# Kernel optimization log

Measured on AMD Instinct MI355X. Metric: run time of the kernel, lower is better.

The kernel has to match this reference:

```python
import jax, jax.numpy as jnp
import numpy as np

B, C, H, W = 4, 128, 64, 64


def setup_inputs() -> dict:
    key = jax.random.key(0)
    ks = jax.random.split(key, 7)
    s = 1.0 / np.sqrt(C)
    return {
        "x": jax.random.normal(ks[0], (B, C, H, W), dtype=jnp.float32),
        "Wq": jax.random.normal(ks[1], (C, C), dtype=jnp.float32) * s,
        "bq": jnp.zeros((C,), dtype=jnp.float32),
        "Wk": jax.random.normal(ks[2], (C, C), dtype=jnp.float32) * s,
        "bk": jnp.zeros((C,), dtype=jnp.float32),
        "Wv": jax.random.normal(ks[3], (C, C), dtype=jnp.float32) * s,
        "bv": jnp.zeros((C,), dtype=jnp.float32),
    }


def reference(x, Wq, bq, Wk, bk, Wv, bv):
    b, c, h, w = x.shape
    n = h * w
    scale = c ** (-0.5)
    # tokens: [B, N, C]
    xt = x.reshape(b, c, n).transpose(0, 2, 1)
    # 1x1 convs == per-token channel GEMMs (out[c'] = sum_c W[c',c] x[c] + b[c'])
    q = jnp.einsum("bnc,dc->bnd", xt, Wq) + bq  # [B, N, C]
    k = jnp.einsum("bnc,dc->bnd", xt, Wk) + bk  # [B, N, C]
    v = jnp.einsum("bnc,dc->bnd", xt, Wv) + bv  # [B, N, C]
    scores = jnp.einsum("bic,bjc->bij", q, k) * scale  # [B, N, N]
    attn = jax.nn.softmax(scores, axis=-1)
    out = jnp.einsum("bij,bjc->bic", attn, v)  # [B, N, C]
    return out.transpose(0, 2, 1).reshape(b, c, h, w)
```

## Files before the change

kernel.cpp:

```cpp
#include <hip/hip_runtime.h>
#include <hip/hip_bf16.h>


#define BATCH 4
#define CH    128
#define NTOK  4096
#define SCALE 0.08838834764831845f
#define LOG2E 1.4426950408889634f
#define MFIX  16.0f

typedef __attribute__((ext_vector_type(8)))  short short8;
typedef __attribute__((ext_vector_type(4)))  float f32x4;
typedef __attribute__((ext_vector_type(16))) float f32x16;

static __device__ __forceinline__ unsigned short f2bf(float f) {
    __hip_bfloat16 h = (__hip_bfloat16)f;
    return *(const unsigned short*)&h;
}

static __device__ __forceinline__ unsigned cvt_pk_bf16(float lo, float hi) {
    unsigned r;
    asm("v_cvt_pk_bf16_f32 %0, %1, %2" : "=v"(r) : "v"(lo), "v"(hi));
    return r;
}

static __device__ __forceinline__ short8 pack_bf16x8(float4 a, float4 b) {
    union { unsigned u[4]; short8 s8; } f;
    f.u[0] = cvt_pk_bf16(a.x, a.y);
    f.u[1] = cvt_pk_bf16(a.z, a.w);
    f.u[2] = cvt_pk_bf16(b.x, b.y);
    f.u[3] = cvt_pk_bf16(b.z, b.w);
    return f.s8;
}

__global__ __launch_bounds__(256) void proj_mfma_kernel(
    const float* __restrict__ x,
    const float* __restrict__ Wq, const float* __restrict__ Wk,
    const float* __restrict__ Wv,
    const float* __restrict__ bq, const float* __restrict__ bk,
    const float* __restrict__ bv,
    unsigned short* __restrict__ q_ws, unsigned short* __restrict__ kf_ws,
    unsigned short* __restrict__ vf_ws)
{
    __shared__ __align__(16) unsigned short Wl[CH * CH];
    __shared__ __align__(16) unsigned short XsT[64 * CH];

    const int t    = threadIdx.x;
    const int w    = t >> 6;
    const int lane = t & 63;
    const int quad = lane >> 4;
    const int c16  = lane & 15;
    const int n0   = blockIdx.x * 64;
    const int b    = blockIdx.y;
    const int z    = blockIdx.z;
    const float* xb = x + (size_t)b * CH * NTOK;
    const float* wm = (z == 0) ? Wq : (z == 1) ? Wk : Wv;

    #pragma unroll
    for (int i = 0; i < 8; ++i) {
        const int f   = i * 256 + t;
        const int row = f >> 4;
        const int u   = f & 15;
        const float* src = wm + f * 8;
        const float4 a = *(const float4*)src;
        const float4 c = *(const float4*)(src + 4);
        *(short8*)&Wl[row * CH + ((u ^ (row & 15)) << 3)] = pack_bf16x8(a, c);
    }
    {
        const int tok = lane;
        #pragma unroll
        for (int cc = 0; cc < 4; ++cc) {
            const int cb = 32 * w + 8 * cc;
            float xv[8];
            #pragma unroll
            for (int j = 0; j < 8; ++j)
                xv[j] = xb[(size_t)(cb + j) * NTOK + n0 + tok];
            union { unsigned u[4]; short8 s8; } pk;
            #pragma unroll
            for (int j = 0; j < 4; ++j)
                pk.u[j] = cvt_pk_bf16(xv[2 * j], xv[2 * j + 1]);
            const int phys = ((cb >> 3) ^ (tok & 15));
            *(short8*)&XsT[tok * CH + phys * 8] = pk.s8;
        }
    }
    __syncthreads();

    if (z < 2) {
        const float* bias = (z == 0) ? bq : bk;
        const float mul = (z == 0) ? (SCALE * LOG2E) : 1.0f;
        short8 xa[4];
        #pragma unroll
        for (int ks = 0; ks < 4; ++ks)
            xa[ks] = *(const short8*)&XsT[(16 * w + c16) * CH + (((4 * ks + quad) ^ c16) << 3)];
        #pragma unroll
        for (int nt = 0; nt < 8; ++nt) {
            f32x4 a = (f32x4){0.f, 0.f, 0.f, 0.f};
            #pragma unroll
            for (int ks = 0; ks < 4; ++ks) {
                const short8 bf = *(const short8*)
                    &Wl[(16 * nt + c16) * CH + (((4 * ks + quad) ^ c16) << 3)];
                a = __builtin_amdgcn_mfma_f32_16x16x32_bf16(xa[ks], bf, a, 0, 0, 0);
            }
            const float bvv = bias[16 * nt + c16];
            #pragma unroll
            for (int r = 0; r < 4; ++r) {
                const int n = n0 + 16 * w + quad * 4 + r;
                if (z == 0) {
                    q_ws[((size_t)b * NTOK + n) * CH + 16 * nt + c16] =
                        f2bf((a[r] + bvv) * mul);
                } else {
                    const size_t idx =
                        (((size_t)b * (NTOK >> 5) + (n >> 5)) * 8 + nt) * 512
                        + ((n & 31) + 32 * (c16 >> 3)) * 8 + (c16 & 7);
                    kf_ws[idx] = f2bf(a[r] + bvv);
                }
            }
        }
    } else {
        #pragma unroll
        for (int nt = 0; nt < 4; ++nt) {
            short8 xbf[4];
            #pragma unroll
            for (int ks = 0; ks < 4; ++ks)
                xbf[ks] = *(const short8*)&XsT[(16 * nt + c16) * CH + (((4 * ks + quad) ^ c16) << 3)];
            #pragma unroll
            for (int mt = 0; mt < 2; ++mt) {
                const int crow16 = 16 * (2 * w + mt);
                f32x4 acc = (f32x4){0.f, 0.f, 0.f, 0.f};
                #pragma unroll
                for (int ks = 0; ks < 4; ++ks) {
                    const short8 wva = *(const short8*)
                        &Wl[(crow16 + c16) * CH + (((4 * ks + quad) ^ c16) << 3)];
                    acc = __builtin_amdgcn_mfma_f32_16x16x32_bf16(wva, xbf[ks], acc, 0, 0, 0);
                }
                #pragma unroll
                for (int r = 0; r < 4; ++r) {
                    const int ch  = crow16 + quad * 4 + r;
                    const int tok = n0 + 16 * nt + c16;
                    const size_t idx =
                        ((((size_t)b * (NTOK >> 5) + (tok >> 5)) * 2
                          + ((tok >> 4) & 1)) * 4 + (ch >> 5)) * 512
                        + ((ch & 31) + 32 * ((tok >> 3) & 1)) * 8 + (tok & 7);
                    vf_ws[idx] = f2bf(acc[r] + bv[ch]);
                }
            }
        }
    }
}

template <int SPLIT>
__global__ __launch_bounds__(256, 2) void flash_attn_mfma(
    const unsigned short* __restrict__ q_ws,
    const unsigned short* __restrict__ kf_ws,
    const unsigned short* __restrict__ vf_ws,
    float* __restrict__ out,
    float* __restrict__ Op, float* __restrict__ l_p)
{
    const int t    = threadIdx.x;
    const int w    = t >> 6;
    const int lane = t & 63;
    const int half = lane >> 5;
    const int l32  = lane & 31;

    int xx, jc, b;
    if constexpr (SPLIT % 2 == 0) {
        const int bid = blockIdx.x;
        b = (bid & 7) >> 1;
        const int sub = (bid & 1) * (16 * SPLIT) + (bid >> 3);
        jc = sub >> 5;
        xx = sub & 31;
    } else {
        const int bid = blockIdx.x;
        xx = bid & 31;
        jc = 0;
        b  = bid >> 5;
    }

    const int n0   = xx * 128;
    const int jbeg = jc * (NTOK / SPLIT);
    constexpr int NT2 = (NTOK / SPLIT) / 32;

    const unsigned short* kg = kf_ws + (size_t)b * NTOK * CH;
    const unsigned short* vg = vf_ws + (size_t)b * NTOK * CH;

    short8 qa[8];
    {
        const unsigned short* qrow =
            q_ws + ((size_t)b * NTOK + n0 + 32 * w + l32) * CH;
        #pragma unroll
        for (int ks = 0; ks < 8; ++ks)
            qa[ks] = *(const short8*)(qrow + ks * 16 + half * 8);
    }

    f32x16 Oa[4];
    #pragma unroll
    for (int ct = 0; ct < 4; ++ct) Oa[ct] = (f32x16)(0.0f);
    float lsum = 0.f;

    short8 kf[8];
    auto KF_LOAD = [&](int jj) {
        const unsigned short* kb = kg + (size_t)(jj >> 5) * (8 * 512);
        #pragma unroll
        for (int ks = 0; ks < 8; ++ks)
            kf[ks] = *(const short8*)(kb + (ks * 64 + lane) * 8);
    };

    KF_LOAD(jbeg);

    int j0 = jbeg;
    for (int tt = 0; tt < NT2; ++tt, j0 += 32) {
        f32x16 s = (f32x16)(-MFIX);
        #pragma unroll
        for (int ks = 0; ks < 8; ++ks)
            s = __builtin_amdgcn_mfma_f32_32x32x16_bf16(kf[ks], qa[ks], s, 0, 0, 0);

        short8 vfA[4], vfB[4];
        {
            const unsigned short* vb = vg + (size_t)(j0 >> 5) * (8 * 512);
            #pragma unroll
            for (int ct = 0; ct < 4; ++ct)
                vfA[ct] = *(const short8*)(vb + ((0 * 4 + ct) * 64 + lane) * 8);
            #pragma unroll
            for (int ct = 0; ct < 4; ++ct)
                vfB[ct] = *(const short8*)(vb + ((1 * 4 + ct) * 64 + lane) * 8);
        }
        if (tt + 1 < NT2) KF_LOAD(j0 + 32);

        float p[16];
        #pragma unroll
        for (int r = 0; r < 16; ++r) p[r] = exp2f(s[r]);
        {
            float a0 = 0.f, a1 = 0.f, a2 = 0.f, a3 = 0.f;
            #pragma unroll
            for (int r = 0; r < 4; ++r) {
                a0 += p[r]; a1 += p[4 + r]; a2 += p[8 + r]; a3 += p[12 + r];
            }
            lsum += (a0 + a1) + (a2 + a3);
        }
        short8 pb0, pb1;
        {
            unsigned wd[8];
            #pragma unroll
            for (int i = 0; i < 8; ++i) wd[i] = cvt_pk_bf16(p[2 * i], p[2 * i + 1]);
            auto r02 = __builtin_amdgcn_permlane32_swap(wd[0], wd[2], false, false);
            auto r13 = __builtin_amdgcn_permlane32_swap(wd[1], wd[3], false, false);
            auto r46 = __builtin_amdgcn_permlane32_swap(wd[4], wd[6], false, false);
            auto r57 = __builtin_amdgcn_permlane32_swap(wd[5], wd[7], false, false);
            union { unsigned u[4]; short8 s8; } f0, f1;
            f0.u[0] = r02[0]; f0.u[1] = r13[0]; f0.u[2] = r02[1]; f0.u[3] = r13[1];
            f1.u[0] = r46[0]; f1.u[1] = r57[0]; f1.u[2] = r46[1]; f1.u[3] = r57[1];
            pb0 = f0.s8;
            pb1 = f1.s8;
        }

        #pragma unroll
        for (int ct = 0; ct < 4; ++ct)
            Oa[ct] = __builtin_amdgcn_mfma_f32_32x32x16_bf16(vfA[ct], pb0, Oa[ct], 0, 0, 0);
        #pragma unroll
        for (int ct = 0; ct < 4; ++ct)
            Oa[ct] = __builtin_amdgcn_mfma_f32_32x32x16_bf16(vfB[ct], pb1, Oa[ct], 0, 0, 0);
    }

    const float lt = lsum + __shfl_xor(lsum, 32);
    const int n = n0 + 32 * w + l32;

    if constexpr (SPLIT == 1) {
        const float inv = 1.0f / lt;
        #pragma unroll
        for (int ct = 0; ct < 4; ++ct) {
            #pragma unroll
            for (int r = 0; r < 16; ++r) {
                const int c = 32 * ct + (r & 3) + 8 * (r >> 2) + 4 * half;
                out[((size_t)b * CH + c) * NTOK + n] = Oa[ct][r] * inv;
            }
        }
    } else {
        const size_t chunk = (size_t)(b * SPLIT + jc);
        #pragma unroll
        for (int ct = 0; ct < 4; ++ct) {
            #pragma unroll
            for (int r = 0; r < 16; ++r) {
                const int c = 32 * ct + (r & 3) + 8 * (r >> 2) + 4 * half;
                Op[(chunk * CH + c) * NTOK + n] = Oa[ct][r];
            }
        }
        if (half == 0) l_p[chunk * NTOK + n] = lt;
    }
}

template <int SPLIT>
__global__ __launch_bounds__(256) void combine_kernel(
    const float* __restrict__ Op, const float* __restrict__ l_p,
    float* __restrict__ out)
{
    const int b = blockIdx.y;
    const size_t idx = ((size_t)blockIdx.x * 256 + threadIdx.x) * 4;
    const int c = (int)(idx >> 12);
    const int n = (int)(idx & (NTOK - 1));
    float4 acc = make_float4(0.f, 0.f, 0.f, 0.f);
    float4 den = make_float4(0.f, 0.f, 0.f, 0.f);
    #pragma unroll
    for (int j = 0; j < SPLIT; ++j) {
        const size_t chunk = (size_t)(b * SPLIT + j);
        const float4 o = *(const float4*)&Op[(chunk * CH + c) * NTOK + n];
        const float4 d = *(const float4*)&l_p[chunk * NTOK + n];
        acc.x += o.x; acc.y += o.y; acc.z += o.z; acc.w += o.w;
        den.x += d.x; den.y += d.y; den.z += d.z; den.w += d.w;
    }
    float4 r;
    r.x = acc.x / den.x; r.y = acc.y / den.y;
    r.z = acc.z / den.z; r.w = acc.w / den.w;
    *(float4*)&out[((size_t)b * CH * NTOK) + idx] = r;
}

extern "C" void kernel_launch(void* const* d_in, const int* in_sizes, int n_in,
                              void* d_out, int out_size, void* d_ws, size_t ws_size,
                              hipStream_t stream) {
    const float* x  = (const float*)d_in[0];
    const float* Wq = (const float*)d_in[1];
    const float* bq = (const float*)d_in[2];
    const float* Wk = (const float*)d_in[3];
    const float* bk = (const float*)d_in[4];
    const float* Wv = (const float*)d_in[5];
    const float* bv = (const float*)d_in[6];
    float* out = (float*)d_out;

    const size_t QKV = (size_t)BATCH * NTOK * CH;
    unsigned short* q_ws  = (unsigned short*)d_ws;
    unsigned short* kf_ws = q_ws + QKV;
    unsigned short* vf_ws = kf_ws + QKV;
    float* Op = (float*)(vf_ws + QKV);

    const size_t baseBytes = 3 * QKV * 2;
    auto needBytes = [&](size_t S) {
        return baseBytes + S * BATCH * NTOK * (size_t)(CH * 4 + 4);
    };

    dim3 gp(NTOK / 64, BATCH, 3);
    proj_mfma_kernel<<<gp, 256, 0, stream>>>(x, Wq, Wk, Wv, bq, bk, bv,
                                             q_ws, kf_ws, vf_ws);

    dim3 gc(CH * NTOK / 1024, BATCH);
    if (ws_size >= needBytes(8)) {
        float* l_p = Op + (size_t)8 * BATCH * NTOK * CH;
        flash_attn_mfma<8><<<dim3(128 * 8), 256, 0, stream>>>(
            q_ws, kf_ws, vf_ws, out, Op, l_p);
        combine_kernel<8><<<gc, 256, 0, stream>>>(Op, l_p, out);
    } else if (ws_size >= needBytes(4)) {
        float* l_p = Op + (size_t)4 * BATCH * NTOK * CH;
        flash_attn_mfma<4><<<dim3(128 * 4), 256, 0, stream>>>(
            q_ws, kf_ws, vf_ws, out, Op, l_p);
        combine_kernel<4><<<gc, 256, 0, stream>>>(Op, l_p, out);
    } else {
        flash_attn_mfma<1><<<dim3(32 * BATCH), 256, 0, stream>>>(
            q_ws, kf_ws, vf_ws, out, nullptr, nullptr);
    }
}
```

Measured before the change: 132.1 us.

## Process two query subtiles per wave to double K/V reuse, stage Q in LDS

Each wave now computes attention for 64 queries (two 32-row subtiles) instead of 32, so each loaded K and V fragment feeds twice as many MFMAs. Q fragments move from registers to shared memory to offset the doubled output accumulators. The second subtile's QK^T and softmax are interleaved with the first's to overlap work. The grid is halved accordingly; this raises register pressure and adds LDS reads, and may reduce occupancy or block-level parallelism.

```diff
diff --git a/kernel.cpp b/kernel.cpp
--- a/kernel.cpp
+++ b/kernel.cpp
@@ -156,6 +156,8 @@
     float* __restrict__ out,
     float* __restrict__ Op, float* __restrict__ l_p)
 {
+    __shared__ __align__(16) unsigned short Ql[4 * 2 * 8 * 64 * 8];
+
     const int t    = threadIdx.x;
     const int w    = t >> 6;
     const int lane = t & 63;
@@ -166,36 +168,41 @@
     if constexpr (SPLIT % 2 == 0) {
         const int bid = blockIdx.x;
         b = (bid & 7) >> 1;
-        const int sub = (bid & 1) * (16 * SPLIT) + (bid >> 3);
-        jc = sub >> 5;
-        xx = sub & 31;
+        const int sub = (bid & 1) * (8 * SPLIT) + (bid >> 3);
+        jc = sub >> 4;
+        xx = sub & 15;
     } else {
-        const int bid = blockIdx.x;
-        xx = bid & 31;
+        xx = blockIdx.x & 15;
         jc = 0;
-        b  = bid >> 5;
-    }
-
-    const int n0   = xx * 128;
+        b  = blockIdx.x >> 4;
+    }
+
+    const int n0   = xx * 256;
     const int jbeg = jc * (NTOK / SPLIT);
     constexpr int NT2 = (NTOK / SPLIT) / 32;
 
     const unsigned short* kg = kf_ws + (size_t)b * NTOK * CH;
     const unsigned short* vg = vf_ws + (size_t)b * NTOK * CH;
 
-    short8 qa[8];
     {
-        const unsigned short* qrow =
-            q_ws + ((size_t)b * NTOK + n0 + 32 * w + l32) * CH;
-        #pragma unroll
-        for (int ks = 0; ks < 8; ++ks)
-            qa[ks] = *(const short8*)(qrow + ks * 16 + half * 8);
-    }
-
-    f32x16 Oa[4];
+        const unsigned short* qbase =
+            q_ws + ((size_t)b * NTOK + n0 + 64 * w) * CH;
+        #pragma unroll
+        for (int qs = 0; qs < 2; ++qs)
+            #pragma unroll
+            for (int ks = 0; ks < 8; ++ks) {
+                const short8 v = *(const short8*)
+                    (qbase + (qs * 32 + l32) * CH + ks * 16 + half * 8);
+                *(short8*)&Ql[(((w * 2 + qs) * 8 + ks) * 64 + lane) * 8] = v;
+            }
+    }
+
+    f32x16 Oa[2][4];
     #pragma unroll
-    for (int ct = 0; ct < 4; ++ct) Oa[ct] = (f32x16)(0.0f);
-    float lsum = 0.f;
+    for (int qs = 0; qs < 2; ++qs)
+        #pragma unroll
+        for (int ct = 0; ct < 4; ++ct) Oa[qs][ct] = (f32x16)(0.0f);
+    float lsum[2] = {0.f, 0.f};
 
     short8 kf[8];
     auto KF_LOAD = [&](int jj) {
@@ -204,15 +211,44 @@
         for (int ks = 0; ks < 8; ++ks)
             kf[ks] = *(const short8*)(kb + (ks * 64 + lane) * 8);
     };
+    auto QKT = [&](int qs, f32x16& s) {
+        #pragma unroll
+        for (int ks = 0; ks < 8; ++ks) {
+            const short8 qf = *(const short8*)
+                &Ql[(((w * 2 + qs) * 8 + ks) * 64 + lane) * 8];
+            s = __builtin_amdgcn_mfma_f32_32x32x16_bf16(kf[ks], qf, s, 0, 0, 0);
+        }
+    };
+    auto SOFTMAX = [&](int qs, const f32x16& s, short8& pb0, short8& pb1) {
+        float p[16];
+        #pragma unroll
+        for (int r = 0; r < 16; ++r) p[r] = exp2f(s[r]);
+        float a0 = 0.f, a1 = 0.f, a2 = 0.f, a3 = 0.f;
+        #pragma unroll
+        for (int r = 0; r < 4; ++r) {
+            a0 += p[r]; a1 += p[4 + r]; a2 += p[8 + r]; a3 += p[12 + r];
+        }
+        lsum[qs] += (a0 + a1) + (a2 + a3);
+        unsigned wd[8];
+        #pragma unroll
+        for (int i = 0; i < 8; ++i) wd[i] = cvt_pk_bf16(p[2 * i], p[2 * i + 1]);
+        auto r02 = __builtin_amdgcn_permlane32_swap(wd[0], wd[2], false, false);
+        auto r13 = __builtin_amdgcn_permlane32_swap(wd[1], wd[3], false, false);
+        auto r46 = __builtin_amdgcn_permlane32_swap(wd[4], wd[6], false, false);
+        auto r57 = __builtin_amdgcn_permlane32_swap(wd[5], wd[7], false, false);
+        union { unsigned u[4]; short8 s8; } f0, f1;
+        f0.u[0] = r02[0]; f0.u[1] = r13[0]; f0.u[2] = r02[1]; f0.u[3] = r13[1];
+        f1.u[0] = r46[0]; f1.u[1] = r57[0]; f1.u[2] = r46[1]; f1.u[3] = r57[1];
+        pb0 = f0.s8;
+        pb1 = f1.s8;
+    };
 
     KF_LOAD(jbeg);
 
     int j0 = jbeg;
     for (int tt = 0; tt < NT2; ++tt, j0 += 32) {
-        f32x16 s = (f32x16)(-MFIX);
-        #pragma unroll
-        for (int ks = 0; ks < 8; ++ks)
-            s = __builtin_amdgcn_mfma_f32_32x32x16_bf16(kf[ks], qa[ks], s, 0, 0, 0);
+        f32x16 s0 = (f32x16)(-MFIX);
+        QKT(0, s0);
 
         short8 vfA[4], vfB[4];
         {
@@ -224,67 +260,56 @@
             for (int ct = 0; ct < 4; ++ct)
                 vfB[ct] = *(const short8*)(vb + ((1 * 4 + ct) * 64 + lane) * 8);
         }
+
+        short8 pb00, pb01;
+        SOFTMAX(0, s0, pb00, pb01);
+
+        f32x16 s1 = (f32x16)(-MFIX);
+        QKT(1, s1);
         if (tt + 1 < NT2) KF_LOAD(j0 + 32);
 
-        float p[16];
-        #pragma unroll
-        for (int r = 0; r < 16; ++r) p[r] = exp2f(s[r]);
-        {
-            float a0 = 0.f, a1 = 0.f, a2 = 0.f, a3 = 0.f;
-            #pragma unroll
-            for (int r = 0; r < 4; ++r) {
-                a0 += p[r]; a1 += p[4 + r]; a2 += p[8 + r]; a3 += p[12 + r];
-            }
-            lsum += (a0 + a1) + (a2 + a3);
-        }
-        short8 pb0, pb1;
-        {
-            unsigned wd[8];
-            #pragma unroll
-            for (int i = 0; i < 8; ++i) wd[i] = cvt_pk_bf16(p[2 * i], p[2 * i + 1]);
-            auto r02 = __builtin_amdgcn_permlane32_swap(wd[0], wd[2], false, false);
-            auto r13 = __builtin_amdgcn_permlane32_swap(wd[1], wd[3], false, false);
-            auto r46 = __builtin_amdgcn_permlane32_swap(wd[4], wd[6], false, false);
-            auto r57 = __builtin_amdgcn_permlane32_swap(wd[5], wd[7], false, false);
-            union { unsigned u[4]; short8 s8; } f0, f1;
-            f0.u[0] = r02[0]; f0.u[1] = r13[0]; f0.u[2] = r02[1]; f0.u[3] = r13[1];
-            f1.u[0] = r46[0]; f1.u[1] = r57[0]; f1.u[2] = r46[1]; f1.u[3] = r57[1];
-            pb0 = f0.s8;
-            pb1 = f1.s8;
-        }
-
-        #pragma unroll
-        for (int ct = 0; ct < 4; ++ct)
-            Oa[ct] = __builtin_amdgcn_mfma_f32_32x32x16_bf16(vfA[ct], pb0, Oa[ct], 0, 0, 0);
-        #pragma unroll
-        for (int ct = 0; ct < 4; ++ct)
-            Oa[ct] = __builtin_amdgcn_mfma_f32_32x32x16_bf16(vfB[ct], pb1, Oa[ct], 0, 0, 0);
-    }
-
-    const float lt = lsum + __shfl_xor(lsum, 32);
-    const int n = n0 + 32 * w + l32;
-
-    if constexpr (SPLIT == 1) {
-        const float inv = 1.0f / lt;
+        short8 pb10, pb11;
+        SOFTMAX(1, s1, pb10, pb11);
+
         #pragma unroll
         for (int ct = 0; ct < 4; ++ct) {
-            #pragma unroll
-            for (int r = 0; r < 16; ++r) {
-                const int c = 32 * ct + (r & 3) + 8 * (r >> 2) + 4 * half;
-                out[((size_t)b * CH + c) * NTOK + n] = Oa[ct][r] * inv;
-            }
-        }
-    } else {
-        const size_t chunk = (size_t)(b * SPLIT + jc);
+            Oa[0][ct] = __builtin_amdgcn_mfma_f32_32x32x16_bf16(vfA[ct], pb00, Oa[0][ct], 0, 0, 0);
+            Oa[1][ct] = __builtin_amdgcn_mfma_f32_32x32x16_bf16(vfA[ct], pb10, Oa[1][ct], 0, 0, 0);
+        }
         #pragma unroll
         for (int ct = 0; ct < 4; ++ct) {
-            #pragma unroll
-            for (int r = 0; r < 16; ++r) {
-                const int c = 32 * ct + (r & 3) + 8 * (r >> 2) + 4 * half;
-                Op[(chunk * CH + c) * NTOK + n] = Oa[ct][r];
-            }
-        }
-        if (half == 0) l_p[chunk * NTOK + n] = lt;
+            Oa[0][ct] = __builtin_amdgcn_mfma_f32_32x32x16_bf16(vfB[ct], pb01, Oa[0][ct], 0, 0, 0);
+            Oa[1][ct] = __builtin_amdgcn_mfma_f32_32x32x16_bf16(vfB[ct], pb11, Oa[1][ct], 0, 0, 0);
+        }
+    }
+
+    #pragma unroll
+    for (int qs = 0; qs < 2; ++qs) {
+        const float lt = lsum[qs] + __shfl_xor(lsum[qs], 32);
+        const int n = n0 + 64 * w + 32 * qs + l32;
+
+        if constexpr (SPLIT == 1) {
+            const float inv = 1.0f / lt;
+            #pragma unroll
+            for (int ct = 0; ct < 4; ++ct) {
+                #pragma unroll
+                for (int r = 0; r < 16; ++r) {
+                    const int c = 32 * ct + (r & 3) + 8 * (r >> 2) + 4 * half;
+                    out[((size_t)b * CH + c) * NTOK + n] = Oa[qs][ct][r] * inv;
+                }
+            }
+        } else {
+            const size_t chunk = (size_t)(b * SPLIT + jc);
+            #pragma unroll
+            for (int ct = 0; ct < 4; ++ct) {
+                #pragma unroll
+                for (int r = 0; r < 16; ++r) {
+                    const int c = 32 * ct + (r & 3) + 8 * (r >> 2) + 4 * half;
+                    Op[(chunk * CH + c) * NTOK + n] = Oa[qs][ct][r];
+                }
+            }
+            if (half == 0) l_p[chunk * NTOK + n] = lt;
+        }
     }
 }
 
@@ -343,16 +368,16 @@
     dim3 gc(CH * NTOK / 1024, BATCH);
     if (ws_size >= needBytes(8)) {
         float* l_p = Op + (size_t)8 * BATCH * NTOK * CH;
-        flash_attn_mfma<8><<<dim3(128 * 8), 256, 0, stream>>>(
+        flash_attn_mfma<8><<<dim3(16 * 8 * BATCH), 256, 0, stream>>>(
             q_ws, kf_ws, vf_ws, out, Op, l_p);
         combine_kernel<8><<<gc, 256, 0, stream>>>(Op, l_p, out);
     } else if (ws_size >= needBytes(4)) {
         float* l_p = Op + (size_t)4 * BATCH * NTOK * CH;
-        flash_attn_mfma<4><<<dim3(128 * 4), 256, 0, stream>>>(
+        flash_attn_mfma<4><<<dim3(16 * 4 * BATCH), 256, 0, stream>>>(
             q_ws, kf_ws, vf_ws, out, Op, l_p);
         combine_kernel<4><<<gc, 256, 0, stream>>>(Op, l_p, out);
     } else {
-        flash_attn_mfma<1><<<dim3(32 * BATCH), 256, 0, stream>>>(
+        flash_attn_mfma<1><<<dim3(16 * BATCH), 256, 0, stream>>>(
             q_ws, kf_ws, vf_ws, out, nullptr, nullptr);
     }
 }
```

Measured after the change: 166.6 us. 1.26x slower.
